# Optimization experiments

Hardware: AMD Instinct MI355X
Metric: run time of the kernel (lower is better)

Reference implementation:

```python
import jax, jax.numpy as jnp
import numpy as np

B, C, H, W = 8, 256, 64, 64
EPS = 1e-5


def _mk_conv_bn(key, oc, ic):
    k = jax.random.split(key, 6)
    return dict(
        w=jax.random.normal(k[0], (oc, ic), jnp.float32) * 0.01,  # trunc-normal approx, stddev 0.01
        b=jnp.zeros((oc,), jnp.float32),
        s=jax.random.uniform(k[1], (oc,), jnp.float32, 0.5, 1.5),   # BN scale
        t=jax.random.normal(k[2], (oc,), jnp.float32) * 0.1,        # BN shift
        m=jax.random.normal(k[3], (oc,), jnp.float32) * 0.1,        # BN running mean
        v=jax.random.uniform(k[4], (oc,), jnp.float32, 0.5, 1.5),   # BN running var
    )


def setup_inputs() -> dict:
    key = jax.random.key(0)
    ks = jax.random.split(key, 6)
    d = {"x": jax.random.normal(ks[0], (B, C, H, W), jnp.float32)}
    for i, (oc, ic) in zip([1, 2, 3, 4], [(C // 8, C), (C // 8, C), (C // 2, C), (C, C // 2)]):
        p = _mk_conv_bn(ks[i], oc, ic)
        for name, val in p.items():
            d[f"{name}{i}"] = val
    d["gamma"] = jnp.asarray(0.5, jnp.float32)
    return d


def _cbn(x, w, b, s, t, m, v, relu=True):
    # conv1x1 + BatchNorm(eval) [+ ReLU]; dropout is identity at inference
    y = jnp.einsum('bchw,oc->bohw', x, w) + b[None, :, None, None]
    scale = (s / jnp.sqrt(v + EPS))[None, :, None, None]
    y = (y - m[None, :, None, None]) * scale + t[None, :, None, None]
    return jax.nn.relu(y) if relu else y


def _maxpool2(x):
    b, c, h, w = x.shape
    return x.reshape(b, c, h // 2, 2, w // 2, 2).max(axis=(3, 5))


def reference(x, w1, b1, s1, t1, m1, v1, w2, b2, s2, t2, m2, v2,
              w3, b3, s3, t3, m3, v3, w4, b4, s4, t4, m4, v4, gamma):
    b, c, h, w = x.shape
    f = _maxpool2(_cbn(x, w1, b1, s1, t1, m1, v1))   # (B, C/8, H/2, W/2)
    g = _cbn(x, w2, b2, s2, t2, m2, v2)              # (B, C/8, H, W)
    hh = _maxpool2(_cbn(x, w3, b3, s3, t3, m3, v3))  # (B, C/2, H/2, W/2)
    hw, hw4 = h * w, (h // 2) * (w // 2)
    f = f.reshape(b, c // 8, hw4).transpose(0, 2, 1)  # (B, HW/4, C/8)
    g = g.reshape(b, c // 8, hw)                      # (B, C/8, HW)
    s = jnp.einsum('bnk,bkm->bnm', f, g)              # (B, HW/4, HW)
    beta = jax.nn.softmax(s, axis=1)                  # softmax over dim=1, as in source
    hh = hh.reshape(b, c // 2, hw4)                   # (B, C/2, HW/4)
    o = jnp.einsum('bcn,bnm->bcm', hh, beta).reshape(b, c // 2, h, w)
    out = _cbn(o, w4, b4, s4, t4, m4, v4, relu=False)
    return gamma * out + x
```

## Files before the change

kernel.cpp:

```cpp
#include <hip/hip_runtime.h>
#include <hip/hip_bf16.h>

#define HW   4096
#define HW4  1024
#define EPS  1e-5f
#define SM_SHIFT 20.0f

typedef __attribute__((ext_vector_type(8))) short bf16x8;
typedef __attribute__((ext_vector_type(4))) float f32x4;

__device__ __forceinline__ short f2bs(float f) {
    union { float f; unsigned u; } v; v.f = f;
    unsigned r = v.u + 0x7FFFu + ((v.u >> 16) & 1u);
    return (short)(r >> 16);
}
__device__ __forceinline__ float bs2f(short s) {
    union { unsigned u; float f; } v; v.u = ((unsigned)(unsigned short)s) << 16;
    return v.f;
}
__device__ __forceinline__ int swz64(int r, int c)  { return (r << 6) + ((c ^ (r & 7))  << 3); }
__device__ __forceinline__ int swz128(int r, int c) { return (r << 7) + ((c ^ (r & 15)) << 3); }
__device__ __forceinline__ int p40(int r, int c)    { return r * 40 + c * 8; }

__global__ __launch_bounds__(256) void conv123pool(
    const float* __restrict__ x,
    const float* __restrict__ w1, const float* __restrict__ b1, const float* __restrict__ s1,
    const float* __restrict__ t1, const float* __restrict__ m1, const float* __restrict__ v1,
    const float* __restrict__ w2, const float* __restrict__ b2, const float* __restrict__ s2,
    const float* __restrict__ t2, const float* __restrict__ m2, const float* __restrict__ v2,
    const float* __restrict__ w3, const float* __restrict__ b3, const float* __restrict__ s3,
    const float* __restrict__ t3, const float* __restrict__ m3, const float* __restrict__ v3,
    short* __restrict__ gbuf, short* __restrict__ fbuf, short* __restrict__ hhbuf)
{
    __shared__ __align__(16) short Wl[192 * 64];
    __shared__ __align__(16) short Xl[128 * 64];
    __shared__ float alB[192], beB[192];

    const int t = threadIdx.x;
    const int lane = t & 63, wv = t >> 6;
    const int quad = lane >> 4, l16 = lane & 15;
    const int ptile = blockIdx.x;
    const int bz = blockIdx.y;
    const int pBase = ptile * 128;

    if (t < 192) {
        int j = t;
        float pb, ps, ptv, pm, pv;
        if (j < 32)      { pb = b1[j]; ps = s1[j]; ptv = t1[j]; pm = m1[j]; pv = v1[j]; }
        else if (j < 64) { int c = j - 32; pb = b2[c]; ps = s2[c]; ptv = t2[c]; pm = m2[c]; pv = v2[c]; }
        else             { int c = j - 64; pb = b3[c]; ps = s3[c]; ptv = t3[c]; pm = m3[c]; pv = v3[c]; }
        float al = ps * rsqrtf(pv + EPS);
        alB[j] = al; beB[j] = (pb - pm) * al + ptv;
    }

    const f32x4 fzero = {0.f, 0.f, 0.f, 0.f};
    f32x4 acc[3][8];
    #pragma unroll
    for (int i = 0; i < 3; ++i)
        #pragma unroll
        for (int j = 0; j < 8; ++j) acc[i][j] = fzero;

    const int xp  = t & 127, xk8 = t >> 7;

    for (int k0 = 0; k0 < 256; k0 += 64) {
        #pragma unroll
        for (int i = 0; i < 3; ++i) {
            int idx = t + i * 256;
            int oc = idx >> 2, kb = (idx & 3) * 16;
            const float* wp = (oc < 32) ? (w1 + oc * 256)
                            : (oc < 64) ? (w2 + (oc - 32) * 256)
                                        : (w3 + (oc - 64) * 256);
            wp += k0 + kb;
            float4 a = *(const float4*)(wp);
            float4 b = *(const float4*)(wp + 4);
            float4 c = *(const float4*)(wp + 8);
            float4 d = *(const float4*)(wp + 12);
            bf16x8 lo, hi;
            lo[0]=f2bs(a.x); lo[1]=f2bs(a.y); lo[2]=f2bs(a.z); lo[3]=f2bs(a.w);
            lo[4]=f2bs(b.x); lo[5]=f2bs(b.y); lo[6]=f2bs(b.z); lo[7]=f2bs(b.w);
            hi[0]=f2bs(c.x); hi[1]=f2bs(c.y); hi[2]=f2bs(c.z); hi[3]=f2bs(c.w);
            hi[4]=f2bs(d.x); hi[5]=f2bs(d.y); hi[6]=f2bs(d.z); hi[7]=f2bs(d.w);
            *(bf16x8*)&Wl[swz64(oc, (kb >> 3))]     = lo;
            *(bf16x8*)&Wl[swz64(oc, (kb >> 3) + 1)] = hi;
        }
        {
            const float* xp0 = x + ((size_t)bz * 256 + k0 + xk8 * 32) * HW + pBase + xp;
            float fv[32];
            #pragma unroll
            for (int i = 0; i < 32; ++i) fv[i] = xp0[(size_t)i * HW];
            #pragma unroll
            for (int c = 0; c < 4; ++c) {
                bf16x8 v;
                #pragma unroll
                for (int jj = 0; jj < 8; ++jj) v[jj] = f2bs(fv[c * 8 + jj]);
                *(bf16x8*)&Xl[swz64(xp, xk8 * 4 + c)] = v;
            }
        }
        __syncthreads();
        #pragma unroll
        for (int kk = 0; kk < 2; ++kk) {
            bf16x8 bfr[8];
            #pragma unroll
            for (int pt = 0; pt < 8; ++pt)
                bfr[pt] = *(const bf16x8*)&Xl[swz64(pt * 16 + l16, kk * 4 + quad)];
            #pragma unroll
            for (int tt = 0; tt < 3; ++tt) {
                bf16x8 afr = *(const bf16x8*)&Wl[swz64(wv * 48 + tt * 16 + l16, kk * 4 + quad)];
                #pragma unroll
                for (int pt = 0; pt < 8; ++pt)
                    acc[tt][pt] = __builtin_amdgcn_mfma_f32_16x16x32_bf16(afr, bfr[pt], acc[tt][pt], 0, 0, 0);
            }
        }
        __syncthreads();
    }

    #pragma unroll
    for (int tt = 0; tt < 3; ++tt) {
        #pragma unroll
        for (int r = 0; r < 4; ++r) {
            int j = wv * 48 + tt * 16 + quad * 4 + r;
            float al = alB[j], be = beB[j];
            float y[8];
            #pragma unroll
            for (int pt = 0; pt < 8; ++pt) y[pt] = fmaxf(acc[tt][pt][r] * al + be, 0.f);
            if (j >= 32 && j < 64) {
                #pragma unroll
                for (int pt = 0; pt < 8; ++pt)
                    gbuf[((size_t)bz * 32 + (j - 32)) * HW + pBase + pt * 16 + l16] = f2bs(y[pt]);
            } else {
                #pragma unroll
                for (int pt = 0; pt < 4; ++pt) {
                    float v  = fmaxf(y[pt], y[pt + 4]);
                    float po = fmaxf(v, __shfl_xor(v, 1));
                    if ((l16 & 1) == 0) {
                        int n = ptile * 32 + ((pt * 16 + l16) >> 1);
                        if (j < 32) fbuf[((size_t)bz * 32 + j) * HW4 + n] = f2bs(po);
                        else        hhbuf[((size_t)bz * 128 + (j - 64)) * HW4 + n] = f2bs(po);
                    }
                }
            }
        }
    }
}

__global__ __launch_bounds__(256, 4) void attn_partial(
    const short* __restrict__ gbuf,
    const short* __restrict__ fbuf,
    const short* __restrict__ hhbuf,
    short* __restrict__ opart,
    float* __restrict__ Zbuf)
{
    __shared__ __align__(16) short smem[17408];
    short* gTl = smem;
    short* fTl = smem + 2560;
    short* sTl = smem + 5120;
    short* hhl = smem + 9216;

    const int t = threadIdx.x;
    const int lane = t & 63, wv = t >> 6;
    const int quad = lane >> 4, l16 = lane & 15;
    const int bz = blockIdx.z;
    const int np = blockIdx.y;
    const int m0 = blockIdx.x * 64;
    const int ms = wv * 16;
    const f32x4 fzero = {0.f, 0.f, 0.f, 0.f};

    {
        int mm = t & 63, k8 = t >> 6;
        bf16x8 v;
        #pragma unroll
        for (int j = 0; j < 8; ++j)
            v[j] = gbuf[((size_t)bz * 32 + k8 * 8 + j) * HW + m0 + mm];
        *(bf16x8*)&gTl[p40(mm, k8)] = v;
    }
    __syncthreads();
    bf16x8 bg = *(const bf16x8*)&gTl[p40(ms + l16, quad)];

    const int fnn = t & 63, fk8 = t >> 6;
    const int hc0 = t >> 3, hnc = t & 7;
    const short* fB = fbuf + (size_t)bz * 32 * HW4;
    const short* hB = hhbuf + (size_t)bz * 128 * HW4;

    float psum = 0.f;
    f32x4 oacc[8];
    #pragma unroll
    for (int i = 0; i < 8; ++i) oacc[i] = fzero;

    const int nbase = np * 512;
    for (int n0 = nbase; n0 < nbase + 512; n0 += 64) {
        __syncthreads();
        {
            bf16x8 v;
            #pragma unroll
            for (int j = 0; j < 8; ++j)
                v[j] = fB[(fk8 * 8 + j) * HW4 + n0 + fnn];
            *(bf16x8*)&fTl[p40(fnn, fk8)] = v;
        }
        {
            #pragma unroll
            for (int i = 0; i < 4; ++i)
                *(bf16x8*)&hhl[swz64(i * 32 + hc0, hnc)] =
                    *(const bf16x8*)(hB + (size_t)(i * 32 + hc0) * HW4 + n0 + hnc * 8);
        }
        __syncthreads();

        f32x4 sacc[4];
        #pragma unroll
        for (int nt = 0; nt < 4; ++nt) {
            bf16x8 af = *(const bf16x8*)&fTl[p40(nt * 16 + l16, quad)];
            sacc[nt] = __builtin_amdgcn_mfma_f32_16x16x32_bf16(af, bg, fzero, 0, 0, 0);
        }

        #pragma unroll
        for (int nt = 0; nt < 4; ++nt) {
            short4 ev;
            #pragma unroll
            for (int r = 0; r < 4; ++r) {
                float e = __expf(sacc[nt][r] - SM_SHIFT);
                psum += e;
                ((short*)&ev)[r] = f2bs(e);
            }
            int chunk = nt * 2 + (quad >> 1);
            *(short4*)&sTl[swz64(ms + l16, chunk) + (quad & 1) * 4] = ev;
        }

        #pragma unroll
        for (int kk = 0; kk < 2; ++kk) {
            bf16x8 bs = *(const bf16x8*)&sTl[swz64(ms + l16, kk * 4 + quad)];
            #pragma unroll
            for (int ct = 0; ct < 8; ++ct) {
                bf16x8 ah = *(const bf16x8*)&hhl[swz64(ct * 16 + l16, kk * 4 + quad)];
                oacc[ct] = __builtin_amdgcn_mfma_f32_16x16x32_bf16(ah, bs, oacc[ct], 0, 0, 0);
            }
        }
    }

    psum += __shfl_xor(psum, 16);
    psum += __shfl_xor(psum, 32);
    int m = m0 + ms + l16;
    if (quad == 0)
        Zbuf[((size_t)bz * 2 + np) * HW + m] = psum;

    #pragma unroll
    for (int ct = 0; ct < 8; ++ct) {
        short4 ov;
        #pragma unroll
        for (int r = 0; r < 4; ++r) ((short*)&ov)[r] = f2bs(oacc[ct][r]);
        *(short4*)(opart + (((size_t)bz * 2 + np) * HW + m) * 128 + ct * 16 + quad * 4) = ov;
    }
}

__global__ __launch_bounds__(256) void conv4_merge(
    const short* __restrict__ opart,
    const float* __restrict__ Zbuf,
    const float* __restrict__ x,
    const float* __restrict__ w4, const float* __restrict__ b4, const float* __restrict__ s4,
    const float* __restrict__ t4, const float* __restrict__ m4, const float* __restrict__ v4,
    const float* __restrict__ gamma, float* __restrict__ out)
{
    __shared__ __align__(16) short smem[24576];
    __shared__ float alB4[256], beB4[256];
    short* o_l = smem;
    short* Wl4 = smem + 8192;

    const int t = threadIdx.x;
    const int lane = t & 63, wv = t >> 6;
    const int quad = lane >> 4, l16 = lane & 15;
    const int bz = blockIdx.y;
    const int m0 = blockIdx.x * 64;
    const f32x4 fzero = {0.f, 0.f, 0.f, 0.f};

    {
        float al = s4[t] * rsqrtf(v4[t] + EPS);
        alB4[t] = al; beB4[t] = (b4[t] - m4[t]) * al + t4[t];
    }

    {
        int m = t >> 2, cb = (t & 3) * 32;
        size_t mi = (size_t)m0 + m;
        const short* p0 = opart + (((size_t)bz * 2 + 0) * HW + mi) * 128 + cb;
        const short* p1 = opart + (((size_t)bz * 2 + 1) * HW + mi) * 128 + cb;
        float z = Zbuf[((size_t)bz * 2 + 0) * HW + mi] + Zbuf[((size_t)bz * 2 + 1) * HW + mi];
        float inv = 1.0f / z;
        #pragma unroll
        for (int seg = 0; seg < 4; ++seg) {
            bf16x8 a = *(const bf16x8*)(p0 + seg * 8);
            bf16x8 b = *(const bf16x8*)(p1 + seg * 8);
            bf16x8 o;
            #pragma unroll
            for (int j = 0; j < 8; ++j)
                o[j] = f2bs((bs2f(a[j]) + bs2f(b[j])) * inv);
            *(bf16x8*)&o_l[swz128(m, (cb >> 3) + seg)] = o;
        }
    }

    f32x4 acc4[4][4];
    #pragma unroll
    for (int i = 0; i < 4; ++i)
        #pragma unroll
        for (int j = 0; j < 4; ++j) acc4[i][j] = fzero;

    for (int c0 = 0; c0 < 128; c0 += 64) {
        #pragma unroll
        for (int i = 0; i < 4; ++i) {
            int oc = i * 64 + (t >> 2);
            int kb = (t & 3) * 16;
            const float* wp = w4 + oc * 128 + c0 + kb;
            float4 a = *(const float4*)(wp);
            float4 b = *(const float4*)(wp + 4);
            float4 c = *(const float4*)(wp + 8);
            float4 d = *(const float4*)(wp + 12);
            bf16x8 lo, hi;
            lo[0]=f2bs(a.x); lo[1]=f2bs(a.y); lo[2]=f2bs(a.z); lo[3]=f2bs(a.w);
            lo[4]=f2bs(b.x); lo[5]=f2bs(b.y); lo[6]=f2bs(b.z); lo[7]=f2bs(b.w);
            hi[0]=f2bs(c.x); hi[1]=f2bs(c.y); hi[2]=f2bs(c.z); hi[3]=f2bs(c.w);
            hi[4]=f2bs(d.x); hi[5]=f2bs(d.y); hi[6]=f2bs(d.z); hi[7]=f2bs(d.w);
            *(bf16x8*)&Wl4[swz64(oc, (kb >> 3))]     = lo;
            *(bf16x8*)&Wl4[swz64(oc, (kb >> 3) + 1)] = hi;
        }
        __syncthreads();
        #pragma unroll
        for (int kk = 0; kk < 2; ++kk) {
            bf16x8 bfr[4];
            #pragma unroll
            for (int mt = 0; mt < 4; ++mt)
                bfr[mt] = *(const bf16x8*)&o_l[swz128(mt * 16 + l16, (c0 >> 3) + kk * 4 + quad)];
            #pragma unroll
            for (int ot = 0; ot < 4; ++ot) {
                bf16x8 afr = *(const bf16x8*)&Wl4[swz64(wv * 64 + ot * 16 + l16, kk * 4 + quad)];
                #pragma unroll
                for (int mt = 0; mt < 4; ++mt)
                    acc4[ot][mt] = __builtin_amdgcn_mfma_f32_16x16x32_bf16(afr, bfr[mt], acc4[ot][mt], 0, 0, 0);
            }
        }
        __syncthreads();
    }

    float gm = gamma[0];
    #pragma unroll
    for (int ot = 0; ot < 4; ++ot) {
        #pragma unroll
        for (int r = 0; r < 4; ++r) {
            int oc = wv * 64 + ot * 16 + quad * 4 + r;
            float al = alB4[oc], be = beB4[oc];
            #pragma unroll
            for (int mt = 0; mt < 4; ++mt) {
                int p = m0 + mt * 16 + l16;
                float y  = acc4[ot][mt][r] * al + be;
                float xo = x[((size_t)bz * 256 + oc) * HW + p];
                out[((size_t)bz * 256 + oc) * HW + p] = gm * y + xo;
            }
        }
    }
}

extern "C" void kernel_launch(void* const* d_in, const int* in_sizes, int n_in,
                              void* d_out, int out_size, void* d_ws, size_t ws_size,
                              hipStream_t stream)
{
    const float* x  = (const float*)d_in[0];
    const float* w1 = (const float*)d_in[1];
    const float* b1 = (const float*)d_in[2];
    const float* s1 = (const float*)d_in[3];
    const float* t1 = (const float*)d_in[4];
    const float* m1 = (const float*)d_in[5];
    const float* v1 = (const float*)d_in[6];
    const float* w2 = (const float*)d_in[7];
    const float* b2 = (const float*)d_in[8];
    const float* s2 = (const float*)d_in[9];
    const float* t2 = (const float*)d_in[10];
    const float* m2 = (const float*)d_in[11];
    const float* v2 = (const float*)d_in[12];
    const float* w3 = (const float*)d_in[13];
    const float* b3 = (const float*)d_in[14];
    const float* s3 = (const float*)d_in[15];
    const float* t3 = (const float*)d_in[16];
    const float* m3 = (const float*)d_in[17];
    const float* v3 = (const float*)d_in[18];
    const float* w4 = (const float*)d_in[19];
    const float* b4 = (const float*)d_in[20];
    const float* s4 = (const float*)d_in[21];
    const float* t4 = (const float*)d_in[22];
    const float* m4 = (const float*)d_in[23];
    const float* v4 = (const float*)d_in[24];
    const float* gm = (const float*)d_in[25];
    float* out = (float*)d_out;

    short* gbuf  = (short*)d_ws;
    short* fbuf  = gbuf  + (size_t)8 * 32 * 4096;
    short* hhbuf = fbuf  + (size_t)8 * 32 * 1024;
    short* opart = hhbuf + (size_t)8 * 128 * 1024;
    float* Zbuf  = (float*)(opart + (size_t)8 * 2 * 4096 * 128);

    conv123pool<<<dim3(32, 8), 256, 0, stream>>>(
        x, w1, b1, s1, t1, m1, v1, w2, b2, s2, t2, m2, v2, w3, b3, s3, t3, m3, v3,
        gbuf, fbuf, hhbuf);
    attn_partial<<<dim3(64, 2, 8), 256, 0, stream>>>(
        gbuf, fbuf, hhbuf, opart, Zbuf);
    conv4_merge<<<dim3(64, 8), 256, 0, stream>>>(
        opart, Zbuf, x, w4, b4, s4, t4, m4, v4, gm, out);
}
```

Baseline: 177.5 us.

## Split conv and attention kernels across output-channel groups for more blocks

The conv123pool kernel is split into two output-channel groups of 96, giving 512 blocks instead of 256. Each wave now covers half the pixel columns and 48 channels, and the accumulator state is halved. The attention partial kernel is split across two halves of the 128 hh channels, doubling its grid, shrinking LDS and accumulators, and raising the occupancy hint from 4 to 5. The aim is better GPU fill and latency hiding. In exchange, x tiles are reloaded twice in conv, and the f/g tiles and S=f·g plus exp are recomputed twice in attention.

```diff
diff --git a/kernel.cpp b/kernel.cpp
--- a/kernel.cpp
+++ b/kernel.cpp
@@ -32,56 +32,63 @@
     const float* __restrict__ t3, const float* __restrict__ m3, const float* __restrict__ v3,
     short* __restrict__ gbuf, short* __restrict__ fbuf, short* __restrict__ hhbuf)
 {
-    __shared__ __align__(16) short Wl[192 * 64];
+    __shared__ __align__(16) short Wl[96 * 64];
     __shared__ __align__(16) short Xl[128 * 64];
-    __shared__ float alB[192], beB[192];
+    __shared__ float alB[96], beB[96];
 
     const int t = threadIdx.x;
     const int lane = t & 63, wv = t >> 6;
     const int quad = lane >> 4, l16 = lane & 15;
     const int ptile = blockIdx.x;
-    const int bz = blockIdx.y;
+    const int ocg   = blockIdx.y;
+    const int bz    = blockIdx.z;
     const int pBase = ptile * 128;
-
-    if (t < 192) {
-        int j = t;
+    const int wcol  = (wv & 1) * 32;
+    const int woch  = (wv >> 1) * 48;
+
+    if (t < 96) {
+        int j = ocg * 96 + t;
         float pb, ps, ptv, pm, pv;
         if (j < 32)      { pb = b1[j]; ps = s1[j]; ptv = t1[j]; pm = m1[j]; pv = v1[j]; }
         else if (j < 64) { int c = j - 32; pb = b2[c]; ps = s2[c]; ptv = t2[c]; pm = m2[c]; pv = v2[c]; }
         else             { int c = j - 64; pb = b3[c]; ps = s3[c]; ptv = t3[c]; pm = m3[c]; pv = v3[c]; }
         float al = ps * rsqrtf(pv + EPS);
-        alB[j] = al; beB[j] = (pb - pm) * al + ptv;
+        alB[t] = al; beB[t] = (pb - pm) * al + ptv;
     }
 
     const f32x4 fzero = {0.f, 0.f, 0.f, 0.f};
-    f32x4 acc[3][8];
+    f32x4 acc[3][4];
     #pragma unroll
     for (int i = 0; i < 3; ++i)
         #pragma unroll
-        for (int j = 0; j < 8; ++j) acc[i][j] = fzero;
-
+        for (int j = 0; j < 4; ++j) acc[i][j] = fzero;
+
+    const int ptOff0 = wcol, ptOff1 = wcol + 16, ptOff2 = wcol + 64, ptOff3 = wcol + 80;
     const int xp  = t & 127, xk8 = t >> 7;
 
     for (int k0 = 0; k0 < 256; k0 += 64) {
         #pragma unroll
-        for (int i = 0; i < 3; ++i) {
+        for (int i = 0; i < 2; ++i) {
             int idx = t + i * 256;
-            int oc = idx >> 2, kb = (idx & 3) * 16;
-            const float* wp = (oc < 32) ? (w1 + oc * 256)
-                            : (oc < 64) ? (w2 + (oc - 32) * 256)
-                                        : (w3 + (oc - 64) * 256);
-            wp += k0 + kb;
-            float4 a = *(const float4*)(wp);
-            float4 b = *(const float4*)(wp + 4);
-            float4 c = *(const float4*)(wp + 8);
-            float4 d = *(const float4*)(wp + 12);
-            bf16x8 lo, hi;
-            lo[0]=f2bs(a.x); lo[1]=f2bs(a.y); lo[2]=f2bs(a.z); lo[3]=f2bs(a.w);
-            lo[4]=f2bs(b.x); lo[5]=f2bs(b.y); lo[6]=f2bs(b.z); lo[7]=f2bs(b.w);
-            hi[0]=f2bs(c.x); hi[1]=f2bs(c.y); hi[2]=f2bs(c.z); hi[3]=f2bs(c.w);
-            hi[4]=f2bs(d.x); hi[5]=f2bs(d.y); hi[6]=f2bs(d.z); hi[7]=f2bs(d.w);
-            *(bf16x8*)&Wl[swz64(oc, (kb >> 3))]     = lo;
-            *(bf16x8*)&Wl[swz64(oc, (kb >> 3) + 1)] = hi;
+            if (i == 0 || t < 128) {
+                int oc = idx >> 2, kb = (idx & 3) * 16;
+                int j = ocg * 96 + oc;
+                const float* wp = (j < 32) ? (w1 + j * 256)
+                                : (j < 64) ? (w2 + (j - 32) * 256)
+                                           : (w3 + (j - 64) * 256);
+                wp += k0 + kb;
+                float4 a = *(const float4*)(wp);
+                float4 b = *(const float4*)(wp + 4);
+                float4 c = *(const float4*)(wp + 8);
+                float4 d = *(const float4*)(wp + 12);
+                bf16x8 lo, hi;
+                lo[0]=f2bs(a.x); lo[1]=f2bs(a.y); lo[2]=f2bs(a.z); lo[3]=f2bs(a.w);
+                lo[4]=f2bs(b.x); lo[5]=f2bs(b.y); lo[6]=f2bs(b.z); lo[7]=f2bs(b.w);
+                hi[0]=f2bs(c.x); hi[1]=f2bs(c.y); hi[2]=f2bs(c.z); hi[3]=f2bs(c.w);
+                hi[4]=f2bs(d.x); hi[5]=f2bs(d.y); hi[6]=f2bs(d.z); hi[7]=f2bs(d.w);
+                *(bf16x8*)&Wl[swz64(oc, (kb >> 3))]     = lo;
+                *(bf16x8*)&Wl[swz64(oc, (kb >> 3) + 1)] = hi;
+            }
         }
         {
             const float* xp0 = x + ((size_t)bz * 256 + k0 + xk8 * 32) * HW + pBase + xp;
@@ -99,15 +106,16 @@
         __syncthreads();
         #pragma unroll
         for (int kk = 0; kk < 2; ++kk) {
-            bf16x8 bfr[8];
-            #pragma unroll
-            for (int pt = 0; pt < 8; ++pt)
-                bfr[pt] = *(const bf16x8*)&Xl[swz64(pt * 16 + l16, kk * 4 + quad)];
+            bf16x8 bfr[4];
+            bfr[0] = *(const bf16x8*)&Xl[swz64(ptOff0 + l16, kk * 4 + quad)];
+            bfr[1] = *(const bf16x8*)&Xl[swz64(ptOff1 + l16, kk * 4 + quad)];
+            bfr[2] = *(const bf16x8*)&Xl[swz64(ptOff2 + l16, kk * 4 + quad)];
+            bfr[3] = *(const bf16x8*)&Xl[swz64(ptOff3 + l16, kk * 4 + quad)];
             #pragma unroll
             for (int tt = 0; tt < 3; ++tt) {
-                bf16x8 afr = *(const bf16x8*)&Wl[swz64(wv * 48 + tt * 16 + l16, kk * 4 + quad)];
+                bf16x8 afr = *(const bf16x8*)&Wl[swz64(woch + tt * 16 + l16, kk * 4 + quad)];
                 #pragma unroll
-                for (int pt = 0; pt < 8; ++pt)
+                for (int pt = 0; pt < 4; ++pt)
                     acc[tt][pt] = __builtin_amdgcn_mfma_f32_16x16x32_bf16(afr, bfr[pt], acc[tt][pt], 0, 0, 0);
             }
         }
@@ -118,22 +126,28 @@
     for (int tt = 0; tt < 3; ++tt) {
         #pragma unroll
         for (int r = 0; r < 4; ++r) {
-            int j = wv * 48 + tt * 16 + quad * 4 + r;
-            float al = alB[j], be = beB[j];
-            float y[8];
-            #pragma unroll
-            for (int pt = 0; pt < 8; ++pt) y[pt] = fmaxf(acc[tt][pt][r] * al + be, 0.f);
+            int ocl = woch + tt * 16 + quad * 4 + r;
+            int j = ocg * 96 + ocl;
+            float al = alB[ocl], be = beB[ocl];
+            float y[4];
+            y[0] = fmaxf(acc[tt][0][r] * al + be, 0.f);
+            y[1] = fmaxf(acc[tt][1][r] * al + be, 0.f);
+            y[2] = fmaxf(acc[tt][2][r] * al + be, 0.f);
+            y[3] = fmaxf(acc[tt][3][r] * al + be, 0.f);
             if (j >= 32 && j < 64) {
-                #pragma unroll
-                for (int pt = 0; pt < 8; ++pt)
-                    gbuf[((size_t)bz * 32 + (j - 32)) * HW + pBase + pt * 16 + l16] = f2bs(y[pt]);
+                size_t base = ((size_t)bz * 32 + (j - 32)) * HW + pBase;
+                gbuf[base + ptOff0 + l16] = f2bs(y[0]);
+                gbuf[base + ptOff1 + l16] = f2bs(y[1]);
+                gbuf[base + ptOff2 + l16] = f2bs(y[2]);
+                gbuf[base + ptOff3 + l16] = f2bs(y[3]);
             } else {
                 #pragma unroll
-                for (int pt = 0; pt < 4; ++pt) {
-                    float v  = fmaxf(y[pt], y[pt + 4]);
+                for (int c = 0; c < 2; ++c) {
+                    float v  = fmaxf(y[c], y[c + 2]);
                     float po = fmaxf(v, __shfl_xor(v, 1));
                     if ((l16 & 1) == 0) {
-                        int n = ptile * 32 + ((pt * 16 + l16) >> 1);
+                        int col = wcol + c * 16 + l16;
+                        int n = ptile * 32 + (col >> 1);
                         if (j < 32) fbuf[((size_t)bz * 32 + j) * HW4 + n] = f2bs(po);
                         else        hhbuf[((size_t)bz * 128 + (j - 64)) * HW4 + n] = f2bs(po);
                     }
@@ -143,14 +157,14 @@
     }
 }
 
-__global__ __launch_bounds__(256, 4) void attn_partial(
+__global__ __launch_bounds__(256, 5) void attn_partial(
     const short* __restrict__ gbuf,
     const short* __restrict__ fbuf,
     const short* __restrict__ hhbuf,
     short* __restrict__ opart,
     float* __restrict__ Zbuf)
 {
-    __shared__ __align__(16) short smem[17408];
+    __shared__ __align__(16) short smem[13312];
     short* gTl = smem;
     short* fTl = smem + 2560;
     short* sTl = smem + 5120;
@@ -160,7 +174,8 @@
     const int lane = t & 63, wv = t >> 6;
     const int quad = lane >> 4, l16 = lane & 15;
     const int bz = blockIdx.z;
-    const int np = blockIdx.y;
+    const int np = blockIdx.y & 1;
+    const int cp = blockIdx.y >> 1;
     const int m0 = blockIdx.x * 64;
     const int ms = wv * 16;
     const f32x4 fzero = {0.f, 0.f, 0.f, 0.f};
@@ -177,14 +192,14 @@
     bf16x8 bg = *(const bf16x8*)&gTl[p40(ms + l16, quad)];
 
     const int fnn = t & 63, fk8 = t >> 6;
-    const int hc0 = t >> 3, hnc = t & 7;
+    const int hrow = t >> 3, hnc = t & 7;
     const short* fB = fbuf + (size_t)bz * 32 * HW4;
-    const short* hB = hhbuf + (size_t)bz * 128 * HW4;
+    const short* hB = hhbuf + ((size_t)bz * 128 + cp * 64) * HW4;
 
     float psum = 0.f;
-    f32x4 oacc[8];
-    #pragma unroll
-    for (int i = 0; i < 8; ++i) oacc[i] = fzero;
+    f32x4 oacc[4];
+    #pragma unroll
+    for (int i = 0; i < 4; ++i) oacc[i] = fzero;
 
     const int nbase = np * 512;
     for (int n0 = nbase; n0 < nbase + 512; n0 += 64) {
@@ -198,9 +213,9 @@
         }
         {
             #pragma unroll
-            for (int i = 0; i < 4; ++i)
-                *(bf16x8*)&hhl[swz64(i * 32 + hc0, hnc)] =
-                    *(const bf16x8*)(hB + (size_t)(i * 32 + hc0) * HW4 + n0 + hnc * 8);
+            for (int i = 0; i < 2; ++i)
+                *(bf16x8*)&hhl[swz64(i * 32 + hrow, hnc)] =
+                    *(const bf16x8*)(hB + (size_t)(i * 32 + hrow) * HW4 + n0 + hnc * 8);
         }
         __syncthreads();
 
@@ -228,7 +243,7 @@
         for (int kk = 0; kk < 2; ++kk) {
             bf16x8 bs = *(const bf16x8*)&sTl[swz64(ms + l16, kk * 4 + quad)];
             #pragma unroll
-            for (int ct = 0; ct < 8; ++ct) {
+            for (int ct = 0; ct < 4; ++ct) {
                 bf16x8 ah = *(const bf16x8*)&hhl[swz64(ct * 16 + l16, kk * 4 + quad)];
                 oacc[ct] = __builtin_amdgcn_mfma_f32_16x16x32_bf16(ah, bs, oacc[ct], 0, 0, 0);
             }
@@ -238,15 +253,15 @@
     psum += __shfl_xor(psum, 16);
     psum += __shfl_xor(psum, 32);
     int m = m0 + ms + l16;
-    if (quad == 0)
+    if (cp == 0 && quad == 0)
         Zbuf[((size_t)bz * 2 + np) * HW + m] = psum;
 
     #pragma unroll
-    for (int ct = 0; ct < 8; ++ct) {
+    for (int ct = 0; ct < 4; ++ct) {
         short4 ov;
         #pragma unroll
         for (int r = 0; r < 4; ++r) ((short*)&ov)[r] = f2bs(oacc[ct][r]);
-        *(short4*)(opart + (((size_t)bz * 2 + np) * HW + m) * 128 + ct * 16 + quad * 4) = ov;
+        *(short4*)(opart + (((size_t)bz * 2 + np) * HW + m) * 128 + cp * 64 + ct * 16 + quad * 4) = ov;
     }
 }
 
@@ -392,10 +407,10 @@
     short* opart = hhbuf + (size_t)8 * 128 * 1024;
     float* Zbuf  = (float*)(opart + (size_t)8 * 2 * 4096 * 128);
 
-    conv123pool<<<dim3(32, 8), 256, 0, stream>>>(
+    conv123pool<<<dim3(32, 2, 8), 256, 0, stream>>>(
         x, w1, b1, s1, t1, m1, v1, w2, b2, s2, t2, m2, v2, w3, b3, s3, t3, m3, v3,
         gbuf, fbuf, hhbuf);
-    attn_partial<<<dim3(64, 2, 8), 256, 0, stream>>>(
+    attn_partial<<<dim3(64, 4, 8), 256, 0, stream>>>(
         gbuf, fbuf, hhbuf, opart, Zbuf);
     conv4_merge<<<dim3(64, 8), 256, 0, stream>>>(
         opart, Zbuf, x, w4, b4, s4, t4, m4, v4, gm, out);
```

Result: no change. 179.3 us (+1.0%).
